# Kernel tuning notes

Measured on AMD Instinct MI355X. Metric: run time of the kernel, lower is better.

The kernel has to match this reference:

```python
import jax, jax.numpy as jnp
import numpy as np

HEADS = 4
DIM_HEAD = 64
SCALE = 8.0
EPS = 1e-5  # fp32 branch of the original LayerNorm


def setup_inputs() -> dict:
    key = jax.random.key(0)
    k1, k2, k3 = jax.random.split(key, 3)
    B, C, F, H, W = 2, 256, 4, 32, 32
    inner = HEADS * DIM_HEAD  # 256
    x = jax.random.normal(k1, (B, C, F, H, W), dtype=jnp.float32)
    gamma = jnp.ones((1, C, 1, 1, 1), dtype=jnp.float32)
    w_qkv = jax.random.normal(k2, (3 * inner, C), dtype=jnp.float32) * 0.05
    w_out = jax.random.normal(k3, (C, inner), dtype=jnp.float32) * 0.05
    return {"x": x, "gamma": gamma, "w_qkv": w_qkv, "w_out": w_out}


def _l2norm(t):
    return t / jnp.sqrt(jnp.sum(t * t, axis=-1, keepdims=True) + 1e-12)


def reference(x, gamma, w_qkv, w_out):
    B, C, F, H, W = x.shape
    N = F * H * W
    inner = HEADS * DIM_HEAD
    residual = x

    # channel LayerNorm (biased variance over dim=1)
    mean = jnp.mean(x, axis=1, keepdims=True)
    var = jnp.mean((x - mean) ** 2, axis=1, keepdims=True)
    xn = (x - mean) / jnp.sqrt(var + EPS) * gamma

    # 1x1x1 conv == channel matmul; flatten spatial dims to sequence
    xn_flat = xn.reshape(B, C, N)                      # [B, C, N]
    qkv = jnp.einsum('oc,bcn->bon', w_qkv, xn_flat)    # [B, 3*inner, N]
    qkv = qkv.reshape(B, 3, HEADS, DIM_HEAD, N)        # chunk then split heads
    qkv = jnp.transpose(qkv, (1, 0, 2, 4, 3))          # [3, B, h, N, d]
    q, k, v = qkv[0], qkv[1], qkv[2]

    q = _l2norm(q)
    k = _l2norm(k)

    sim = jnp.einsum('bhid,bhjd->bhij', q, k) * SCALE  # [B, h, N, N]
    attn = jax.nn.softmax(sim, axis=-1)
    out = jnp.einsum('bhij,bhjd->bhid', attn, v)       # [B, h, N, d]

    # 'b h n d -> b (h d) n' then 1x1x1 out conv
    out = jnp.transpose(out, (0, 1, 3, 2)).reshape(B, inner, N)
    out = jnp.einsum('oi,bin->bon', w_out, out).reshape(B, C, F, H, W)
    return out + residual
```

## Files before the change

### kernel.cpp

```cpp
#include <hip/hip_runtime.h>

#define BATCH 2
#define CCH   256
#define NSEQ  4096
#define NH    4
#define DH    64
#define INNER 256

typedef __attribute__((ext_vector_type(8))) __bf16 bf16x8;
typedef __attribute__((ext_vector_type(4))) float f32x4;
typedef __attribute__((ext_vector_type(8))) unsigned short u16x8;
typedef __attribute__((ext_vector_type(4))) unsigned short u16x4;

#define GLD16(gsrc, ldst)                                                     \
  __builtin_amdgcn_global_load_lds(                                           \
      (const __attribute__((address_space(1))) unsigned int*)(const void*)(gsrc), \
      (__attribute__((address_space(3))) unsigned int*)(void*)(ldst), 16, 0, 0)

static __device__ __forceinline__ unsigned short f2bfr(float f) {
  union { float f; unsigned u; } v; v.f = f;
  return (unsigned short)((v.u + 0x8000u) >> 16);
}
static __device__ __forceinline__ unsigned pack2(float f0, float f1) {
  union { float f; unsigned u; } a, b; a.f = f0; b.f = f1;
  return __builtin_amdgcn_perm(b.u + 0x8000u, a.u + 0x8000u, 0x07060302u);
}
static __device__ __forceinline__ unsigned cvtpk(float lo, float hi) {
  unsigned r;
  asm("v_cvt_pk_bf16_f32 %0, %1, %2" : "=v"(r) : "v"(lo), "v"(hi));
  return r;
}
static __device__ __forceinline__ float bf2f(unsigned short u) {
  union { unsigned u; float f; } v; v.u = ((unsigned)u) << 16;
  return v.f;
}
static __device__ __forceinline__ bf16x8 ldb(const unsigned short* p) {
  return *(const bf16x8*)p;
}
static __device__ __forceinline__ f32x4 mm(bf16x8 a, bf16x8 b, f32x4 c) {
  return __builtin_amdgcn_mfma_f32_16x16x32_bf16(a, b, c, 0, 0, 0);
}
static __device__ __forceinline__ float ex2(float x) {
  return __builtin_amdgcn_exp2f(x);
}

__global__ __launch_bounds__(256) void k_lncvt(const float* __restrict__ x,
                                               const float* __restrict__ gamma,
                                               unsigned short* __restrict__ xn,
                                               const float* __restrict__ wq,
                                               const float* __restrict__ wo,
                                               unsigned short* __restrict__ wqb,
                                               unsigned short* __restrict__ wob) {
  int blk = blockIdx.x;
  if (blk >= 256) {
    int t = (blk - 256) * 256 + threadIdx.x;
    int e = t * 4;
    if (e < 768 * 256) {
      float4 v = *(const float4*)(wq + e);
      u16x4 pk = { f2bfr(v.x), f2bfr(v.y), f2bfr(v.z), f2bfr(v.w) };
      *(u16x4*)(wqb + e) = pk;
    } else {
      int e2 = e - 768 * 256;
      float4 v = *(const float4*)(wo + e2);
      u16x4 pk = { f2bfr(v.x), f2bfr(v.y), f2bfr(v.z), f2bfr(v.w) };
      *(u16x4*)(wob + e2) = pk;
    }
    return;
  }
  int b  = blk >> 7;
  int n0 = (blk & 127) * 32;
  int t  = threadIdx.x;
  int nl = t & 31;
  int cg = t >> 5;
  int n  = n0 + nl;
  const float* xp = x + ((size_t)(b * CCH + cg * 32)) * NSEQ + n;
  float vals[32];
  float s = 0.f, s2 = 0.f;
#pragma unroll
  for (int j = 0; j < 32; j++) {
    float v = xp[(size_t)j * NSEQ];
    vals[j] = v; s += v; s2 += v * v;
  }
  __shared__ float rs[8][32], rs2[8][32];
  rs[cg][nl] = s; rs2[cg][nl] = s2;
  __syncthreads();
  float S = 0.f, S2 = 0.f;
#pragma unroll
  for (int g = 0; g < 8; g++) { S += rs[g][nl]; S2 += rs2[g][nl]; }
  float mean = S * (1.f / 256.f);
  float var  = S2 * (1.f / 256.f) - mean * mean;
  float rstd = rsqrtf(var + 1e-5f);
  unsigned short* dst = xn + ((size_t)b * NSEQ + n) * CCH + cg * 32;
#pragma unroll
  for (int j0 = 0; j0 < 32; j0 += 8) {
    u16x8 pk;
#pragma unroll
    for (int j = 0; j < 8; j++)
      pk[j] = f2bfr((vals[j0 + j] - mean) * rstd * gamma[cg * 32 + j0 + j]);
    *(u16x8*)(dst + j0) = pk;
  }
}

__global__ __launch_bounds__(256) void k_qkv(const unsigned short* __restrict__ wqb,
                                             const unsigned short* __restrict__ xn,
                                             unsigned short* __restrict__ qkv,
                                             unsigned short* __restrict__ qt,
                                             unsigned short* __restrict__ ktb) {
  int n0 = blockIdx.x * 64;
  int oi = blockIdx.y;
  int o0 = oi * 64;
  int b  = blockIdx.z;
  __shared__ unsigned short Al[64 * 128];
  __shared__ unsigned short Bl[64 * 128];
  int t = threadIdx.x;
  int lane = t & 63, w = t >> 6;
  int c = lane & 15, quad = lane >> 4;
  int wm = w >> 1, wn = w & 1;
  f32x4 acc[2][2] = {};
  int lr = lane >> 4;
  int lchk = lane & 15;
  const unsigned short* apg = wqb + (size_t)o0 * CCH;
  const unsigned short* bpg = xn + ((size_t)b * NSEQ + n0) * CCH;
  for (int kt = 0; kt < 2; kt++) {
    if (kt) __syncthreads();
#pragma unroll
    for (int q = 0; q < 4; q++) {
      int r = w * 16 + q * 4 + lr;
      int srcoff = r * CCH + kt * 128 + ((lchk ^ (r & 7)) * 8);
      GLD16(apg + srcoff, Al + (size_t)(w * 16 + q * 4) * 128);
      GLD16(bpg + srcoff, Bl + (size_t)(w * 16 + q * 4) * 128);
    }
    __syncthreads();
#pragma unroll
    for (int ks = 0; ks < 4; ks++) {
      int ra0 = wm * 32 + c, ra1 = ra0 + 16;
      int rb0 = wn * 32 + c, rb1 = rb0 + 16;
      bf16x8 a0 = ldb(&Al[ra0 * 128 + (((ks * 4 + quad) ^ (ra0 & 7)) * 8)]);
      bf16x8 a1 = ldb(&Al[ra1 * 128 + (((ks * 4 + quad) ^ (ra1 & 7)) * 8)]);
      bf16x8 b0 = ldb(&Bl[rb0 * 128 + (((ks * 4 + quad) ^ (rb0 & 7)) * 8)]);
      bf16x8 b1 = ldb(&Bl[rb1 * 128 + (((ks * 4 + quad) ^ (rb1 & 7)) * 8)]);
      acc[0][0] = mm(a0, b0, acc[0][0]);
      acc[0][1] = mm(a0, b1, acc[0][1]);
      acc[1][0] = mm(a1, b0, acc[1][0]);
      acc[1][1] = mm(a1, b1, acc[1][1]);
    }
  }
  if (oi < 8) {
    float* sq = (float*)Al;
    float s0 = 0.f, s1 = 0.f;
#pragma unroll
    for (int i = 0; i < 2; i++)
#pragma unroll
      for (int rr = 0; rr < 4; rr++) {
        s0 += acc[i][0][rr] * acc[i][0][rr];
        s1 += acc[i][1][rr] * acc[i][1][rr];
      }
    s0 += __shfl_xor(s0, 16); s0 += __shfl_xor(s0, 32);
    s1 += __shfl_xor(s1, 16); s1 += __shfl_xor(s1, 32);
    __syncthreads();
    if (quad == 0) {
      sq[wm * 64 + wn * 32 + c]      = s0;
      sq[wm * 64 + wn * 32 + 16 + c] = s1;
    }
    __syncthreads();
    float r0 = rsqrtf(sq[wn * 32 + c]      + sq[64 + wn * 32 + c]      + 1e-12f);
    float r1 = rsqrtf(sq[wn * 32 + 16 + c] + sq[64 + wn * 32 + 16 + c] + 1e-12f);
    if (oi < 4) { r0 *= 11.541560327111707f; r1 *= 11.541560327111707f; }
    int h = oi & 3;
    unsigned short* base = (oi < 4 ? qt : ktb) + ((size_t)(b * NH + h) * NSEQ) * DH;
#pragma unroll
    for (int i = 0; i < 2; i++)
#pragma unroll
      for (int j = 0; j < 2; j++) {
        float rsc = j ? r1 : r0;
        int n = n0 + wn * 32 + j * 16 + c;
        int d = wm * 32 + i * 16 + quad * 4;
        uint2 pk = { pack2(acc[i][j][0] * rsc, acc[i][j][1] * rsc),
                     pack2(acc[i][j][2] * rsc, acc[i][j][3] * rsc) };
        *(uint2*)(base + (size_t)n * DH + d) = pk;
      }
  } else {
#pragma unroll
    for (int i = 0; i < 2; i++)
#pragma unroll
      for (int j = 0; j < 2; j++)
#pragma unroll
        for (int rr = 0; rr < 4; rr++) {
          int o = o0 + wm * 32 + i * 16 + quad * 4 + rr;
          int n = n0 + wn * 32 + j * 16 + c;
          qkv[((size_t)b * 768 + o) * NSEQ + n] = f2bfr(acc[i][j][rr]);
        }
  }
}

__global__ __launch_bounds__(256, 4) void k_attn(
    const unsigned short* __restrict__ qt,
    const unsigned short* __restrict__ ktb,
    const unsigned short* __restrict__ qkv,
    unsigned short* __restrict__ opart,
    float* __restrict__ lpart,
    int S, int kvlen) {
  int i0 = blockIdx.x * 128;
  int h  = blockIdx.y;
  int bz = blockIdx.z;
  int b  = bz / S, s = bz % S;
  __shared__ unsigned short Kl[2][64 * 64];
  __shared__ unsigned short Vl[2][64 * 64];
  int t = threadIdx.x;
  int lane = t & 63, w = t >> 6;
  int c = lane & 15, quad = lane >> 4;

  const unsigned short* qbase = qt  + ((size_t)(b * NH + h) * NSEQ) * DH;
  const unsigned short* kbase = ktb + ((size_t)(b * NH + h) * NSEQ) * DH;
  const unsigned short* vbase = qkv + ((size_t)b * 768 + 512 + h * 64) * NSEQ;

  int rlo = w * 32 + c, rhi = rlo + 16;
  const unsigned short* qlo = qbase + (size_t)(i0 + rlo) * DH + quad * 8;
  const unsigned short* qhi = qlo + 16 * DH;
  bf16x8 qlo0 = ldb(qlo), qlo1 = ldb(qlo + 32);
  bf16x8 qhi0 = ldb(qhi), qhi1 = ldb(qhi + 32);

  u16x8 onesu;
#pragma unroll
  for (int j = 0; j < 8; j++) onesu[j] = 0x3F80;
  bf16x8 ones = *(bf16x8*)&onesu;

  f32x4 acclo[4] = {}, acchi[4] = {};
  f32x4 accllo = {}, acclhi = {};

  int slr = lane >> 3, slc = lane & 7;
  int ssw_v  = (slc ^ slr) * 8;
  int ssw_k1 = (slc ^ (slr & 3)) * 8;
  int ssw_k2 = ssw_k1 ^ 32;
  const unsigned short* kp = kbase + (size_t)(s * kvlen + w * 16 + slr) * DH;
  const unsigned short* vp = vbase + (size_t)(w * 16 + slr) * NSEQ + s * kvlen + ssw_v;
  int sw0 = (quad ^ (c & 7)) * 8;
  int sw1 = sw0 ^ 32;
  int fK    = (c & 3) | (((c >> 2) & 1) << 2);
  int swk0  = (quad ^ fK) * 8;
  int swk1  = swk0 ^ 32;
  int krow0 = (c >> 2) * 8 + (c & 3);

  int nIt = kvlen / 64;
  GLD16(kp + ssw_k1,          &Kl[0][(w * 16)     * 64]);
  GLD16(kp + 8 * DH + ssw_k2, &Kl[0][(w * 16 + 8) * 64]);
  GLD16(vp,                   &Vl[0][(w * 16)     * 64]);
  GLD16(vp + 8 * NSEQ,        &Vl[0][(w * 16 + 8) * 64]);
  kp += 64 * DH; vp += 64;

  union U4 { unsigned u[4]; bf16x8 v; };

  for (int it = 0; it < nIt; it++) {
    int cur = it & 1;
    __syncthreads();
    if (it + 1 < nIt) {
      int nb = cur ^ 1;
      GLD16(kp + ssw_k1,          &Kl[nb][(w * 16)     * 64]);
      GLD16(kp + 8 * DH + ssw_k2, &Kl[nb][(w * 16 + 8) * 64]);
      GLD16(vp,                   &Vl[nb][(w * 16)     * 64]);
      GLD16(vp + 8 * NSEQ,        &Vl[nb][(w * 16 + 8) * 64]);
      kp += 64 * DH; vp += 64;
    }

    const unsigned short* Kb = &Kl[cur][0];
    bf16x8 k00 = ldb(&Kb[(krow0)      * 64 + swk0]);
    bf16x8 k01 = ldb(&Kb[(krow0)      * 64 + swk1]);
    bf16x8 k10 = ldb(&Kb[(krow0 + 4)  * 64 + swk0]);
    bf16x8 k11 = ldb(&Kb[(krow0 + 4)  * 64 + swk1]);
    bf16x8 k20 = ldb(&Kb[(krow0 + 32) * 64 + swk0]);
    bf16x8 k21 = ldb(&Kb[(krow0 + 32) * 64 + swk1]);
    bf16x8 k30 = ldb(&Kb[(krow0 + 36) * 64 + swk0]);
    bf16x8 k31 = ldb(&Kb[(krow0 + 36) * 64 + swk1]);

    U4 plo0, plo1, phi0, phi1;
    {
      __builtin_amdgcn_s_setprio(1);
      f32x4 zl0 = {}; zl0 = mm(k00, qlo0, zl0); zl0 = mm(k01, qlo1, zl0);
      f32x4 zh0 = {}; zh0 = mm(k00, qhi0, zh0); zh0 = mm(k01, qhi1, zh0);
      f32x4 zl1 = {}; zl1 = mm(k10, qlo0, zl1); zl1 = mm(k11, qlo1, zl1);
      f32x4 zh1 = {}; zh1 = mm(k10, qhi0, zh1); zh1 = mm(k11, qhi1, zh1);
      __builtin_amdgcn_s_setprio(0);
      plo0.u[0] = cvtpk(ex2(zl0[0]), ex2(zl0[1]));
      plo0.u[1] = cvtpk(ex2(zl0[2]), ex2(zl0[3]));
      plo0.u[2] = cvtpk(ex2(zl1[0]), ex2(zl1[1]));
      plo0.u[3] = cvtpk(ex2(zl1[2]), ex2(zl1[3]));
      phi0.u[0] = cvtpk(ex2(zh0[0]), ex2(zh0[1]));
      phi0.u[1] = cvtpk(ex2(zh0[2]), ex2(zh0[3]));
      phi0.u[2] = cvtpk(ex2(zh1[0]), ex2(zh1[1]));
      phi0.u[3] = cvtpk(ex2(zh1[2]), ex2(zh1[3]));
    }
    {
      __builtin_amdgcn_s_setprio(1);
      f32x4 zl2 = {}; zl2 = mm(k20, qlo0, zl2); zl2 = mm(k21, qlo1, zl2);
      f32x4 zh2 = {}; zh2 = mm(k20, qhi0, zh2); zh2 = mm(k21, qhi1, zh2);
      f32x4 zl3 = {}; zl3 = mm(k30, qlo0, zl3); zl3 = mm(k31, qlo1, zl3);
      f32x4 zh3 = {}; zh3 = mm(k30, qhi0, zh3); zh3 = mm(k31, qhi1, zh3);
      __builtin_amdgcn_s_setprio(0);
      plo1.u[0] = cvtpk(ex2(zl2[0]), ex2(zl2[1]));
      plo1.u[1] = cvtpk(ex2(zl2[2]), ex2(zl2[3]));
      plo1.u[2] = cvtpk(ex2(zl3[0]), ex2(zl3[1]));
      plo1.u[3] = cvtpk(ex2(zl3[2]), ex2(zl3[3]));
      phi1.u[0] = cvtpk(ex2(zh2[0]), ex2(zh2[1]));
      phi1.u[1] = cvtpk(ex2(zh2[2]), ex2(zh2[3]));
      phi1.u[2] = cvtpk(ex2(zh3[0]), ex2(zh3[1]));
      phi1.u[3] = cvtpk(ex2(zh3[2]), ex2(zh3[3]));
    }

#pragma unroll
    for (int dt = 0; dt < 4; dt++) {
      bf16x8 v0 = ldb(&Vl[cur][(dt * 16 + c) * 64 + sw0]);
      bf16x8 v1 = ldb(&Vl[cur][(dt * 16 + c) * 64 + sw1]);
      __builtin_amdgcn_s_setprio(1);
      acclo[dt] = mm(plo0.v, v0, acclo[dt]);
      acclo[dt] = mm(plo1.v, v1, acclo[dt]);
      acchi[dt] = mm(phi0.v, v0, acchi[dt]);
      acchi[dt] = mm(phi1.v, v1, acchi[dt]);
      __builtin_amdgcn_s_setprio(0);
    }
    __builtin_amdgcn_s_setprio(1);
    accllo = mm(plo0.v, ones, accllo); accllo = mm(plo1.v, ones, accllo);
    acclhi = mm(phi0.v, ones, acclhi); acclhi = mm(phi1.v, ones, acclhi);
    __builtin_amdgcn_s_setprio(0);
  }

  size_t rb = ((size_t)(b * NH + h) * S + s) * NSEQ + i0 + w * 32;
  if (c == 0) {
#pragma unroll
    for (int rr = 0; rr < 4; rr++) {
      lpart[rb + quad * 4 + rr]      = accllo[rr];
      lpart[rb + 16 + quad * 4 + rr] = acclhi[rr];
    }
  }
#pragma unroll
  for (int rr = 0; rr < 4; rr++)
#pragma unroll
    for (int dt = 0; dt < 4; dt++) {
      opart[(rb + quad * 4 + rr) * 64 + dt * 16 + c]      = f2bfr(acclo[dt][rr]);
      opart[(rb + 16 + quad * 4 + rr) * 64 + dt * 16 + c] = f2bfr(acchi[dt][rr]);
    }
}

__global__ __launch_bounds__(256) void k_merge(
    const unsigned short* __restrict__ opart,
    const float* __restrict__ lpart,
    unsigned short* __restrict__ ao, int S) {
  int t = blockIdx.x * 256 + threadIdx.x;
  int row = t >> 2;
  int dseg = (t & 3) * 16;
  int b = row >> 14, rem = row & 16383;
  int h = rem >> 12, i = rem & 4095;

  float l = 0.f;
  float o[16];
#pragma unroll
  for (int j = 0; j < 16; j++) o[j] = 0.f;
  for (int s = 0; s < S; s++) {
    size_t rb = ((size_t)(b * NH + h) * S + s) * NSEQ + i;
    l += lpart[rb];
    const unsigned short* p = opart + rb * 64 + dseg;
    u16x8 v0 = *(const u16x8*)p;
    u16x8 v1 = *(const u16x8*)(p + 8);
#pragma unroll
    for (int j = 0; j < 8; j++) {
      o[j]     += bf2f(v0[j]);
      o[8 + j] += bf2f(v1[j]);
    }
  }
  float inv = 1.f / l;
  unsigned short* dst = ao + ((size_t)b * NSEQ + i) * INNER + h * 64 + dseg;
  uint4 pk0 = { pack2(o[0] * inv, o[1] * inv),  pack2(o[2] * inv, o[3] * inv),
                pack2(o[4] * inv, o[5] * inv),  pack2(o[6] * inv, o[7] * inv) };
  uint4 pk1 = { pack2(o[8] * inv, o[9] * inv),  pack2(o[10] * inv, o[11] * inv),
                pack2(o[12] * inv, o[13] * inv),pack2(o[14] * inv, o[15] * inv) };
  *(uint4*)dst = pk0;
  *(uint4*)(dst + 8) = pk1;
}

__global__ __launch_bounds__(256) void k_out(const unsigned short* __restrict__ wob,
                                             const unsigned short* __restrict__ ao,
                                             const float* __restrict__ x,
                                             float* __restrict__ out) {
  int n0 = blockIdx.x * 64;
  int o0 = blockIdx.y * 64;
  int b  = blockIdx.z;
  __shared__ unsigned short Al[64 * 128];
  __shared__ unsigned short Bl[64 * 128];
  int t = threadIdx.x;
  int lane = t & 63, w = t >> 6;
  int c = lane & 15, quad = lane >> 4;
  int wm = w >> 1, wn = w & 1;
  f32x4 acc[2][2] = {};
  int lr = lane >> 4;
  int lchk = lane & 15;
  const unsigned short* apg = wob + (size_t)o0 * INNER;
  const unsigned short* bpg = ao + ((size_t)b * NSEQ + n0) * INNER;
  for (int kt = 0; kt < 2; kt++) {
    if (kt) __syncthreads();
#pragma unroll
    for (int q = 0; q < 4; q++) {
      int r = w * 16 + q * 4 + lr;
      int srcoff = r * INNER + kt * 128 + ((lchk ^ (r & 7)) * 8);
      GLD16(apg + srcoff, Al + (size_t)(w * 16 + q * 4) * 128);
      GLD16(bpg + srcoff, Bl + (size_t)(w * 16 + q * 4) * 128);
    }
    __syncthreads();
#pragma unroll
    for (int ks = 0; ks < 4; ks++) {
      int ra0 = wm * 32 + c, ra1 = ra0 + 16;
      int rb0 = wn * 32 + c, rb1 = rb0 + 16;
      bf16x8 a0 = ldb(&Al[ra0 * 128 + (((ks * 4 + quad) ^ (ra0 & 7)) * 8)]);
      bf16x8 a1 = ldb(&Al[ra1 * 128 + (((ks * 4 + quad) ^ (ra1 & 7)) * 8)]);
      bf16x8 b0 = ldb(&Bl[rb0 * 128 + (((ks * 4 + quad) ^ (rb0 & 7)) * 8)]);
      bf16x8 b1 = ldb(&Bl[rb1 * 128 + (((ks * 4 + quad) ^ (rb1 & 7)) * 8)]);
      acc[0][0] = mm(a0, b0, acc[0][0]);
      acc[0][1] = mm(a0, b1, acc[0][1]);
      acc[1][0] = mm(a1, b0, acc[1][0]);
      acc[1][1] = mm(a1, b1, acc[1][1]);
    }
  }
#pragma unroll
  for (int i = 0; i < 2; i++)
#pragma unroll
    for (int j = 0; j < 2; j++)
#pragma unroll
      for (int rr = 0; rr < 4; rr++) {
        int o = o0 + wm * 32 + i * 16 + quad * 4 + rr;
        int n = n0 + wn * 32 + j * 16 + c;
        size_t idx = ((size_t)b * CCH + o) * NSEQ + n;
        out[idx] = acc[i][j][rr] + x[idx];
      }
}

extern "C" void kernel_launch(void* const* d_in, const int* in_sizes, int n_in,
                              void* d_out, int out_size, void* d_ws, size_t ws_size,
                              hipStream_t stream) {
  const float* x     = (const float*)d_in[0];
  const float* gamma = (const float*)d_in[1];
  const float* wq    = (const float*)d_in[2];
  const float* wo    = (const float*)d_in[3];
  float* out = (float*)d_out;

  const size_t MB = 1u << 20;
  char* ws = (char*)d_ws;
  unsigned short* ao  = (unsigned short*)ws;
  unsigned short* xn  = (unsigned short*)(ws + 4 * MB);
  unsigned short* qkv = (unsigned short*)(ws + 8 * MB);
  unsigned short* wqb = (unsigned short*)(ws + 20 * MB);
  unsigned short* wob = (unsigned short*)(ws + 20 * MB + 512 * 1024);
  unsigned short* qt  = (unsigned short*)(ws + 21 * MB);
  unsigned short* ktb = (unsigned short*)(ws + 25 * MB);
  unsigned short* opart = (unsigned short*)(ws + 29 * MB);
  int S;
  if (ws_size >= 48 * MB) S = 4;
  else if (ws_size >= 40 * MB) S = 2;
  else S = 1;
  size_t opart_bytes = (size_t)S * BATCH * NH * NSEQ * DH * 2;
  float* lpart = (float*)(ws + 29 * MB + opart_bytes);
  int kvlen = NSEQ / S;

  k_lncvt<<<dim3(512),          256, 0, stream>>>(x, gamma, xn, wq, wo, wqb, wob);
  k_qkv  <<<dim3(64, 12, 2),    256, 0, stream>>>(wqb, xn, qkv, qt, ktb);
  k_attn <<<dim3(32, 4, 2 * S), 256, 0, stream>>>(qt, ktb, qkv, opart,
                                                  lpart, S, kvlen);
  k_merge<<<dim3(512),          256, 0, stream>>>(opart, lpart, ao, S);
  k_out  <<<dim3(64, 4, 2),     256, 0, stream>>>(wob, ao, x, out);
}
```

Measured before the change: 126.9 us.

## Double query rows per attention block to reuse K/V tiles across more queries

```diff
diff --git a/kernel.cpp b/kernel.cpp
--- a/kernel.cpp
+++ b/kernel.cpp
@@ -193,14 +193,14 @@
   }
 }
 
-__global__ __launch_bounds__(256, 4) void k_attn(
+__global__ __launch_bounds__(256, 2) void k_attn(
     const unsigned short* __restrict__ qt,
     const unsigned short* __restrict__ ktb,
     const unsigned short* __restrict__ qkv,
     unsigned short* __restrict__ opart,
     float* __restrict__ lpart,
     int S, int kvlen) {
-  int i0 = blockIdx.x * 128;
+  int i0 = blockIdx.x * 256;
   int h  = blockIdx.y;
   int bz = blockIdx.z;
   int b  = bz / S, s = bz % S;
@@ -214,19 +214,21 @@
   const unsigned short* kbase = ktb + ((size_t)(b * NH + h) * NSEQ) * DH;
   const unsigned short* vbase = qkv + ((size_t)b * 768 + 512 + h * 64) * NSEQ;
 
-  int rlo = w * 32 + c, rhi = rlo + 16;
-  const unsigned short* qlo = qbase + (size_t)(i0 + rlo) * DH + quad * 8;
-  const unsigned short* qhi = qlo + 16 * DH;
-  bf16x8 qlo0 = ldb(qlo), qlo1 = ldb(qlo + 32);
-  bf16x8 qhi0 = ldb(qhi), qhi1 = ldb(qhi + 32);
+  bf16x8 qa[4], qb[4];
+#pragma unroll
+  for (int ss = 0; ss < 4; ss++) {
+    const unsigned short* qp =
+        qbase + (size_t)(i0 + w * 64 + ss * 16 + c) * DH + quad * 8;
+    qa[ss] = ldb(qp); qb[ss] = ldb(qp + 32);
+  }
 
   u16x8 onesu;
 #pragma unroll
   for (int j = 0; j < 8; j++) onesu[j] = 0x3F80;
   bf16x8 ones = *(bf16x8*)&onesu;
 
-  f32x4 acclo[4] = {}, acchi[4] = {};
-  f32x4 accllo = {}, acclhi = {};
+  f32x4 acc[4][4] = {};
+  f32x4 accl[4]  = {};
 
   int slr = lane >> 3, slc = lane & 7;
   int ssw_v  = (slc ^ slr) * 8;
@@ -249,6 +251,26 @@
   kp += 64 * DH; vp += 64;
 
   union U4 { unsigned u[4]; bf16x8 v; };
+  U4 p0[4], p1[4];
+
+#define QKSET(qA, qB, P0, P1)                                                 \
+  {                                                                           \
+    f32x4 z0 = {}, z1 = {}, z2 = {}, z3 = {};                                 \
+    __builtin_amdgcn_s_setprio(1);                                            \
+    z0 = mm(k00, qA, z0); z0 = mm(k01, qB, z0);                               \
+    z1 = mm(k10, qA, z1); z1 = mm(k11, qB, z1);                               \
+    z2 = mm(k20, qA, z2); z2 = mm(k21, qB, z2);                               \
+    z3 = mm(k30, qA, z3); z3 = mm(k31, qB, z3);                               \
+    __builtin_amdgcn_s_setprio(0);                                            \
+    P0.u[0] = cvtpk(ex2(z0[0]), ex2(z0[1]));                                  \
+    P0.u[1] = cvtpk(ex2(z0[2]), ex2(z0[3]));                                  \
+    P0.u[2] = cvtpk(ex2(z1[0]), ex2(z1[1]));                                  \
+    P0.u[3] = cvtpk(ex2(z1[2]), ex2(z1[3]));                                  \
+    P1.u[0] = cvtpk(ex2(z2[0]), ex2(z2[1]));                                  \
+    P1.u[1] = cvtpk(ex2(z2[2]), ex2(z2[3]));                                  \
+    P1.u[2] = cvtpk(ex2(z3[0]), ex2(z3[1]));                                  \
+    P1.u[3] = cvtpk(ex2(z3[2]), ex2(z3[3]));                                  \
+  }
 
   for (int it = 0; it < nIt; it++) {
     int cur = it & 1;
@@ -272,72 +294,48 @@
     bf16x8 k30 = ldb(&Kb[(krow0 + 36) * 64 + swk0]);
     bf16x8 k31 = ldb(&Kb[(krow0 + 36) * 64 + swk1]);
 
-    U4 plo0, plo1, phi0, phi1;
-    {
-      __builtin_amdgcn_s_setprio(1);
-      f32x4 zl0 = {}; zl0 = mm(k00, qlo0, zl0); zl0 = mm(k01, qlo1, zl0);
-      f32x4 zh0 = {}; zh0 = mm(k00, qhi0, zh0); zh0 = mm(k01, qhi1, zh0);
-      f32x4 zl1 = {}; zl1 = mm(k10, qlo0, zl1); zl1 = mm(k11, qlo1, zl1);
-      f32x4 zh1 = {}; zh1 = mm(k10, qhi0, zh1); zh1 = mm(k11, qhi1, zh1);
-      __builtin_amdgcn_s_setprio(0);
-      plo0.u[0] = cvtpk(ex2(zl0[0]), ex2(zl0[1]));
-      plo0.u[1] = cvtpk(ex2(zl0[2]), ex2(zl0[3]));
-      plo0.u[2] = cvtpk(ex2(zl1[0]), ex2(zl1[1]));
-      plo0.u[3] = cvtpk(ex2(zl1[2]), ex2(zl1[3]));
-      phi0.u[0] = cvtpk(ex2(zh0[0]), ex2(zh0[1]));
-      phi0.u[1] = cvtpk(ex2(zh0[2]), ex2(zh0[3]));
-      phi0.u[2] = cvtpk(ex2(zh1[0]), ex2(zh1[1]));
-      phi0.u[3] = cvtpk(ex2(zh1[2]), ex2(zh1[3]));
-    }
-    {
-      __builtin_amdgcn_s_setprio(1);
-      f32x4 zl2 = {}; zl2 = mm(k20, qlo0, zl2); zl2 = mm(k21, qlo1, zl2);
-      f32x4 zh2 = {}; zh2 = mm(k20, qhi0, zh2); zh2 = mm(k21, qhi1, zh2);
-      f32x4 zl3 = {}; zl3 = mm(k30, qlo0, zl3); zl3 = mm(k31, qlo1, zl3);
-      f32x4 zh3 = {}; zh3 = mm(k30, qhi0, zh3); zh3 = mm(k31, qhi1, zh3);
-      __builtin_amdgcn_s_setprio(0);
-      plo1.u[0] = cvtpk(ex2(zl2[0]), ex2(zl2[1]));
-      plo1.u[1] = cvtpk(ex2(zl2[2]), ex2(zl2[3]));
-      plo1.u[2] = cvtpk(ex2(zl3[0]), ex2(zl3[1]));
-      plo1.u[3] = cvtpk(ex2(zl3[2]), ex2(zl3[3]));
-      phi1.u[0] = cvtpk(ex2(zh2[0]), ex2(zh2[1]));
-      phi1.u[1] = cvtpk(ex2(zh2[2]), ex2(zh2[3]));
-      phi1.u[2] = cvtpk(ex2(zh3[0]), ex2(zh3[1]));
-      phi1.u[3] = cvtpk(ex2(zh3[2]), ex2(zh3[3]));
-    }
+    QKSET(qa[0], qb[0], p0[0], p1[0]);
+    QKSET(qa[1], qb[1], p0[1], p1[1]);
+    QKSET(qa[2], qb[2], p0[2], p1[2]);
+    QKSET(qa[3], qb[3], p0[3], p1[3]);
 
 #pragma unroll
     for (int dt = 0; dt < 4; dt++) {
       bf16x8 v0 = ldb(&Vl[cur][(dt * 16 + c) * 64 + sw0]);
       bf16x8 v1 = ldb(&Vl[cur][(dt * 16 + c) * 64 + sw1]);
       __builtin_amdgcn_s_setprio(1);
-      acclo[dt] = mm(plo0.v, v0, acclo[dt]);
-      acclo[dt] = mm(plo1.v, v1, acclo[dt]);
-      acchi[dt] = mm(phi0.v, v0, acchi[dt]);
-      acchi[dt] = mm(phi1.v, v1, acchi[dt]);
+#pragma unroll
+      for (int ss = 0; ss < 4; ss++) {
+        acc[ss][dt] = mm(p0[ss].v, v0, acc[ss][dt]);
+        acc[ss][dt] = mm(p1[ss].v, v1, acc[ss][dt]);
+      }
       __builtin_amdgcn_s_setprio(0);
     }
     __builtin_amdgcn_s_setprio(1);
-    accllo = mm(plo0.v, ones, accllo); accllo = mm(plo1.v, ones, accllo);
-    acclhi = mm(phi0.v, ones, acclhi); acclhi = mm(phi1.v, ones, acclhi);
+#pragma unroll
+    for (int ss = 0; ss < 4; ss++) {
+      accl[ss] = mm(p0[ss].v, ones, accl[ss]);
+      accl[ss] = mm(p1[ss].v, ones, accl[ss]);
+    }
     __builtin_amdgcn_s_setprio(0);
   }
-
-  size_t rb = ((size_t)(b * NH + h) * S + s) * NSEQ + i0 + w * 32;
-  if (c == 0) {
-#pragma unroll
-    for (int rr = 0; rr < 4; rr++) {
-      lpart[rb + quad * 4 + rr]      = accllo[rr];
-      lpart[rb + 16 + quad * 4 + rr] = acclhi[rr];
-    }
-  }
-#pragma unroll
-  for (int rr = 0; rr < 4; rr++)
-#pragma unroll
-    for (int dt = 0; dt < 4; dt++) {
-      opart[(rb + quad * 4 + rr) * 64 + dt * 16 + c]      = f2bfr(acclo[dt][rr]);
-      opart[(rb + 16 + quad * 4 + rr) * 64 + dt * 16 + c] = f2bfr(acchi[dt][rr]);
-    }
+#undef QKSET
+
+  size_t rb = ((size_t)(b * NH + h) * S + s) * NSEQ + i0 + w * 64;
+#pragma unroll
+  for (int ss = 0; ss < 4; ss++) {
+    size_t rbs = rb + ss * 16;
+    if (c == 0) {
+#pragma unroll
+      for (int rr = 0; rr < 4; rr++)
+        lpart[rbs + quad * 4 + rr] = accl[ss][rr];
+    }
+#pragma unroll
+    for (int rr = 0; rr < 4; rr++)
+#pragma unroll
+      for (int dt = 0; dt < 4; dt++)
+        opart[(rbs + quad * 4 + rr) * 64 + dt * 16 + c] = f2bfr(acc[ss][dt][rr]);
+  }
 }
 
 __global__ __launch_bounds__(256) void k_merge(
@@ -460,7 +458,7 @@
 
   k_lncvt<<<dim3(512),          256, 0, stream>>>(x, gamma, xn, wq, wo, wqb, wob);
   k_qkv  <<<dim3(64, 12, 2),    256, 0, stream>>>(wqb, xn, qkv, qt, ktb);
-  k_attn <<<dim3(32, 4, 2 * S), 256, 0, stream>>>(qt, ktb, qkv, opart,
+  k_attn <<<dim3(16, 4, 2 * S), 256, 0, stream>>>(qt, ktb, qkv, opart,
                                                   lpart, S, kvlen);
   k_merge<<<dim3(512),          256, 0, stream>>>(opart, lpart, ao, S);
   k_out  <<<dim3(64, 4, 2),     256, 0, stream>>>(wob, ao, x, out);
```

New measurement: 124.0 us. 1.02x faster.
